# Optimization experiments

Hardware: AMD Instinct MI355X
Metric: run time of the kernel (lower is better)

## Reference

```python
import jax, jax.numpy as jnp
import numpy as np

N = 65536          # number of atoms (routing tokens)
NUM_SPECIES = 4    # number of per-species expert models
D_IN, D_HID, D_OUT = 256, 1024, 256


def setup_inputs() -> dict:
    key = jax.random.key(0)
    k = jax.random.split(key, 6)
    x = jax.random.normal(k[0], (N, D_IN), dtype=jnp.float32)
    central_species = jax.random.randint(k[1], (N,), 0, NUM_SPECIES, dtype=jnp.int64)
    # Per-species 2-layer MLP experts, stacked along species axis.
    W1 = jax.random.normal(k[2], (NUM_SPECIES, D_IN, D_HID), dtype=jnp.float32) * (1.0 / np.sqrt(D_IN))
    b1 = jnp.zeros((NUM_SPECIES, D_HID), dtype=jnp.float32)
    W2 = jax.random.normal(k[3], (NUM_SPECIES, D_HID, D_OUT), dtype=jnp.float32) * (1.0 / np.sqrt(D_HID))
    b2 = jnp.zeros((NUM_SPECIES, D_OUT), dtype=jnp.float32)
    return {"x": x, "central_species": central_species, "W1": W1, "b1": b1, "W2": W2, "b2": b2}


def reference(x, central_species, W1, b1, W2, b2):
    # Equivalent to: split rows by species (CentralSplitter), apply the
    # species-specific submodel, scatter results back by mask (CentralUniter).
    # Dense-compute-and-select expression: every row receives exactly the
    # output of its own species' expert, identical math to masked gather/scatter.
    num_species = W1.shape[0]
    out = jnp.zeros((x.shape[0], W2.shape[-1]), dtype=x.dtype)
    for s in range(num_species):  # small fixed expert count
        h = jax.nn.silu(x @ W1[s] + b1[s])          # [N, D_HID]
        y = h @ W2[s] + b2[s]                       # [N, D_OUT]
        sel = (central_species == s)[:, None]
        out = out + jnp.where(sel, y, jnp.zeros_like(y))
    return out
```

## Files before the change

kernel.cpp:

```cpp
#include <hip/hip_runtime.h>
#include <hip/hip_bf16.h>


#define N_ATOMS 65536
#define D_IN 256
#define D_HID 1024
#define D_OUT 256
#define TPS 1024

typedef __attribute__((ext_vector_type(8))) short short8;
typedef __attribute__((ext_vector_type(4))) short short4v;
typedef __attribute__((ext_vector_type(4))) float float4e;
typedef __attribute__((ext_vector_type(2))) unsigned uint2e;
typedef __attribute__((ext_vector_type(4))) unsigned uint4e;

#define WS_BUCKET_OFF 256
#define WS_W1_OFF 1048832
#define WS_W2_OFF 3145984

__device__ __forceinline__ short f2bf(float f) {
  unsigned u = __builtin_bit_cast(unsigned, f);
  unsigned r = (u + 0x7FFFu + ((u >> 16) & 1u)) >> 16;
  return (short)r;
}

__device__ __forceinline__ unsigned cvt_pk_bf16(float a, float b) {
  unsigned r;
  asm("v_cvt_pk_bf16_f32 %0, %1, %2" : "=v"(r) : "v"(a), "v"(b));
  return r;
}

__global__ void prep_kernel(const float* __restrict__ W1, const float* __restrict__ W2,
                            short* __restrict__ w1sw, short* __restrict__ w2sw,
                            int* __restrict__ cnt) {
  int gid = blockIdx.x * 256 + threadIdx.x;
  if (gid < 64) cnt[gid] = 0;
  int lane = gid & 63;
  int lr = lane & 15;
  int lk = (lane >> 4) * 8;
  if (gid < 131072) {
    int ks = (gid >> 6) & 7;
    int nt = (gid >> 9) & 63;
    int s  = gid >> 15;
    const float* src = W1 + ((size_t)(s * 256 + ks * 32 + lk)) * 1024 + nt * 16 + lr;
    short8 v;
    for (int j = 0; j < 8; ++j) v[j] = f2bf(src[(size_t)j * 1024]);
    *(short8*)(w1sw + (size_t)gid * 8) = v;
  } else {
    int g = gid - 131072;
    int kt = (g >> 6) & 31;
    int nt = (g >> 11) & 15;
    int s  = g >> 15;
    const float* src = W2 + ((size_t)(s * 1024 + kt * 32 + lk)) * 256 + nt * 16 + lr;
    short8 v;
    for (int j = 0; j < 8; ++j) v[j] = f2bf(src[(size_t)j * 256]);
    *(short8*)(w2sw + (size_t)g * 8) = v;
  }
}

#define CF_BLOCKS 32
#define CF_ITERS 8
__global__ void count_fill_kernel(const int* __restrict__ species,
                                  int* __restrict__ cnt, int* __restrict__ bucket) {
  int tid = threadIdx.x;
  int lane = tid & 63, wid = tid >> 6;
  __shared__ int wcnt[CF_ITERS][4][4];
  __shared__ int wb[CF_ITERS][4][4];
  __shared__ int base_sm[4];
  int sv[CF_ITERS], rk[CF_ITERS];
  unsigned long long below = (1ull << lane) - 1ull;
  int base_i = blockIdx.x * (CF_ITERS * 256);
  #pragma unroll
  for (int it = 0; it < CF_ITERS; ++it) {
    int s = species[base_i + it * 256 + tid] & 3;
    sv[it] = s;
    unsigned long long m0 = __ballot(s == 0);
    unsigned long long m1 = __ballot(s == 1);
    unsigned long long m2 = __ballot(s == 2);
    unsigned long long m3 = __ballot(s == 3);
    unsigned long long ms = (s == 0) ? m0 : (s == 1) ? m1 : (s == 2) ? m2 : m3;
    rk[it] = __popcll(ms & below);
    if (lane == 0) {
      wcnt[it][wid][0] = __popcll(m0);
      wcnt[it][wid][1] = __popcll(m1);
      wcnt[it][wid][2] = __popcll(m2);
      wcnt[it][wid][3] = __popcll(m3);
    }
  }
  __syncthreads();
  if (tid < 4) {
    int ss = tid, run = 0;
    for (int it = 0; it < CF_ITERS; ++it)
      for (int w = 0; w < 4; ++w) {
        wb[it][w][ss] = run;
        run += wcnt[it][w][ss];
      }
    base_sm[ss] = atomicAdd(&cnt[ss * 16], run);
  }
  __syncthreads();
  #pragma unroll
  for (int it = 0; it < CF_ITERS; ++it) {
    int ss = sv[it];
    bucket[ss * N_ATOMS + base_sm[ss] + wb[it][wid][ss] + rk[it]] = base_i + it * 256 + tid;
  }
}

#define XS_STRIDE 280
#define HS_STRIDE 152
__global__ __launch_bounds__(256, 2) void fused_kernel(
    const float* __restrict__ x, const int* __restrict__ cntArr,
    const int* __restrict__ bucket, const short* __restrict__ w1sw,
    const short* __restrict__ w2sw, const float* __restrict__ b1,
    const float* __restrict__ b2, float* __restrict__ out) {
  int bid = blockIdx.x;
  int s = (bid & 7) >> 1;
  int t = ((bid >> 3) << 1) | (bid & 1);
  int cnt = cntArr[s * 16];
  int r0 = t * 64;
  if (r0 >= cnt) return;
  int nrows = min(64, cnt - r0);
  const int* buck = bucket + s * N_ATOMS + r0;

  __shared__ short Xs[64 * XS_STRIDE];
  __shared__ short Hs[2][64 * HS_STRIDE];

  int tid = threadIdx.x;

  for (int i = 0; i < 8; ++i) {
    int id = tid + i * 256;
    int r = id >> 5;
    int g = id & 31;
    float4 f0 = {}, f1 = {};
    if (r < nrows) {
      const float4* src = (const float4*)(x + (size_t)buck[r] * D_IN + g * 8);
      f0 = src[0];
      f1 = src[1];
    }
    uint4e v;
    v.x = cvt_pk_bf16(f0.x, f0.y);
    v.y = cvt_pk_bf16(f0.z, f0.w);
    v.z = cvt_pk_bf16(f1.x, f1.y);
    v.w = cvt_pk_bf16(f1.z, f1.w);
    *(uint4e*)(Xs + r * XS_STRIDE + g * 8) = v;
  }

  int lane = tid & 63;
  int wid = tid >> 6;
  int lr = lane & 15;
  int lk = (lane >> 4) * 8;
  int lq = (lane >> 4) * 4;

  int rowIdx[4];
  #pragma unroll
  for (int bt = 0; bt < 4; ++bt) {
    int r = bt * 16 + lr;
    rowIdx[bt] = (r < nrows) ? buck[r] : -1;
  }

  float4e accY[4][4];
  #pragma unroll
  for (int at = 0; at < 4; ++at) {
    float4e bv = *(const float4e*)(b2 + s * D_OUT + wid * 64 + at * 16 + lq);
    #pragma unroll
    for (int bt = 0; bt < 4; ++bt) accY[at][bt] = bv;
  }

  short8 b1f[16];
  #pragma unroll
  for (int ks = 0; ks < 8; ++ks)
    #pragma unroll
    for (int at = 0; at < 2; ++at) {
      int nt = 0 * 8 + wid * 2 + at;
      b1f[ks * 2 + at] = *(const short8*)(w1sw + ((size_t)((s * 64 + nt) * 8 + ks)) * 512 + lane * 8);
    }

  __syncthreads();

  for (int c = 0; c < 8; ++c) {
    float4e acc1[2][4];
    #pragma unroll
    for (int at = 0; at < 2; ++at) {
      float4e bv = *(const float4e*)(b1 + s * D_HID + c * 128 + wid * 32 + at * 16 + lq);
      #pragma unroll
      for (int bt = 0; bt < 4; ++bt) acc1[at][bt] = bv;
    }
    __builtin_amdgcn_s_setprio(1);
    #pragma unroll
    for (int ks = 0; ks < 8; ++ks) {
      short8 xb[4];
      #pragma unroll
      for (int bt = 0; bt < 4; ++bt)
        xb[bt] = *(const short8*)(Xs + (bt * 16 + lr) * XS_STRIDE + ks * 32 + lk);
      #pragma unroll
      for (int at = 0; at < 2; ++at)
        #pragma unroll
        for (int bt = 0; bt < 4; ++bt)
          acc1[at][bt] = __builtin_amdgcn_mfma_f32_16x16x32_bf16(b1f[ks * 2 + at], xb[bt], acc1[at][bt], 0, 0, 0);
    }
    __builtin_amdgcn_s_setprio(0);
    short8 b2f[16];
    #pragma unroll
    for (int ks = 0; ks < 4; ++ks)
      #pragma unroll
      for (int at = 0; at < 4; ++at) {
        int nt = wid * 4 + at;
        int kt = c * 4 + ks;
        b2f[ks * 4 + at] = *(const short8*)(w2sw + ((size_t)((s * 16 + nt) * 32 + kt)) * 512 + lane * 8);
      }
    short* hsb = Hs[c & 1];
    #pragma unroll
    for (int at = 0; at < 2; ++at) {
      int hidloc = wid * 32 + at * 16 + lq;
      #pragma unroll
      for (int bt = 0; bt < 4; ++bt) {
        float4e v4 = acc1[at][bt];
        float sv0 = v4[0] * __builtin_amdgcn_rcpf(1.0f + __expf(-v4[0]));
        float sv1 = v4[1] * __builtin_amdgcn_rcpf(1.0f + __expf(-v4[1]));
        float sv2 = v4[2] * __builtin_amdgcn_rcpf(1.0f + __expf(-v4[2]));
        float sv3 = v4[3] * __builtin_amdgcn_rcpf(1.0f + __expf(-v4[3]));
        uint2e h;
        h.x = cvt_pk_bf16(sv0, sv1);
        h.y = cvt_pk_bf16(sv2, sv3);
        *(uint2e*)(hsb + (bt * 16 + lr) * HS_STRIDE + hidloc) = h;
      }
    }
    __syncthreads();
    if (c < 7) {
      #pragma unroll
      for (int ks = 0; ks < 8; ++ks)
        #pragma unroll
        for (int at = 0; at < 2; ++at) {
          int nt = (c + 1) * 8 + wid * 2 + at;
          b1f[ks * 2 + at] = *(const short8*)(w1sw + ((size_t)((s * 64 + nt) * 8 + ks)) * 512 + lane * 8);
        }
    }
    __builtin_amdgcn_s_setprio(1);
    #pragma unroll
    for (int ks = 0; ks < 4; ++ks) {
      short8 hb[4];
      #pragma unroll
      for (int bt = 0; bt < 4; ++bt)
        hb[bt] = *(const short8*)(hsb + (bt * 16 + lr) * HS_STRIDE + ks * 32 + lk);
      #pragma unroll
      for (int at = 0; at < 4; ++at)
        #pragma unroll
        for (int bt = 0; bt < 4; ++bt)
          accY[at][bt] = __builtin_amdgcn_mfma_f32_16x16x32_bf16(b2f[ks * 4 + at], hb[bt], accY[at][bt], 0, 0, 0);
    }
    __builtin_amdgcn_s_setprio(0);
  }

  #pragma unroll
  for (int at = 0; at < 4; ++at) {
    int nb = wid * 64 + at * 16 + lq;
    #pragma unroll
    for (int bt = 0; bt < 4; ++bt) {
      if (rowIdx[bt] >= 0)
        *(float4e*)(out + (size_t)rowIdx[bt] * D_OUT + nb) = accY[at][bt];
    }
  }
}

extern "C" void kernel_launch(void* const* d_in, const int* in_sizes, int n_in,
                              void* d_out, int out_size, void* d_ws, size_t ws_size,
                              hipStream_t stream) {
  const float* x  = (const float*)d_in[0];
  const int* spc  = (const int*)d_in[1];
  const float* W1 = (const float*)d_in[2];
  const float* b1 = (const float*)d_in[3];
  const float* W2 = (const float*)d_in[4];
  const float* b2 = (const float*)d_in[5];
  float* out = (float*)d_out;

  int*   cnt    = (int*)d_ws;
  int*   bucket = (int*)((char*)d_ws + WS_BUCKET_OFF);
  short* w1sw   = (short*)((char*)d_ws + WS_W1_OFF);
  short* w2sw   = (short*)((char*)d_ws + WS_W2_OFF);

  prep_kernel<<<1024, 256, 0, stream>>>(W1, W2, w1sw, w2sw, cnt);
  count_fill_kernel<<<CF_BLOCKS, 256, 0, stream>>>(spc, cnt, bucket);
  fused_kernel<<<4 * TPS, 256, 0, stream>>>(x, cnt, bucket, w1sw, w2sw, b1, b2, out);
}
```

Before: 219.9 us.

## Merge weight prep and species bucketing into one kernel launch

```diff
diff --git a/kernel.cpp b/kernel.cpp
--- a/kernel.cpp
+++ b/kernel.cpp
@@ -9,7 +9,6 @@
 #define TPS 1024
 
 typedef __attribute__((ext_vector_type(8))) short short8;
-typedef __attribute__((ext_vector_type(4))) short short4v;
 typedef __attribute__((ext_vector_type(4))) float float4e;
 typedef __attribute__((ext_vector_type(2))) unsigned uint2e;
 typedef __attribute__((ext_vector_type(4))) unsigned uint4e;
@@ -17,6 +16,10 @@
 #define WS_BUCKET_OFF 256
 #define WS_W1_OFF 1048832
 #define WS_W2_OFF 3145984
+
+#define CF_BLOCKS 32
+#define CF_ITERS 8
+#define CF_ROWS (CF_ITERS * 256)
 
 __device__ __forceinline__ short f2bf(float f) {
   unsigned u = __builtin_bit_cast(unsigned, f);
@@ -30,11 +33,77 @@
   return r;
 }
 
-__global__ void prep_kernel(const float* __restrict__ W1, const float* __restrict__ W2,
-                            short* __restrict__ w1sw, short* __restrict__ w2sw,
-                            int* __restrict__ cnt) {
-  int gid = blockIdx.x * 256 + threadIdx.x;
-  if (gid < 64) cnt[gid] = 0;
+__global__ __launch_bounds__(256) void prep_count_kernel(
+    const float* __restrict__ W1, const float* __restrict__ W2,
+    short* __restrict__ w1sw, short* __restrict__ w2sw,
+    const int* __restrict__ species, int* __restrict__ cnt,
+    int* __restrict__ bucket) {
+  int tid = threadIdx.x;
+
+  if (blockIdx.x < CF_BLOCKS) {
+    __shared__ int red[4];
+    __shared__ int wcnt[CF_ITERS][4][4];
+    __shared__ int wb[CF_ITERS][4][4];
+    int b = blockIdx.x;
+    if (tid < 4) red[tid] = 0;
+    __syncthreads();
+
+    int pc0 = 0, pc1 = 0, pc2 = 0, pc3 = 0;
+    int nPrefix = b * CF_ROWS;
+    for (int base = tid * 4; base < nPrefix; base += 1024) {
+      int4 v = *(const int4*)(species + base);
+      int s0 = v.x & 3, s1 = v.y & 3, s2 = v.z & 3, s3 = v.w & 3;
+      pc0 += (s0 == 0) + (s1 == 0) + (s2 == 0) + (s3 == 0);
+      pc1 += (s0 == 1) + (s1 == 1) + (s2 == 1) + (s3 == 1);
+      pc2 += (s0 == 2) + (s1 == 2) + (s2 == 2) + (s3 == 2);
+      pc3 += (s0 == 3) + (s1 == 3) + (s2 == 3) + (s3 == 3);
+    }
+    if (pc0) atomicAdd(&red[0], pc0);
+    if (pc1) atomicAdd(&red[1], pc1);
+    if (pc2) atomicAdd(&red[2], pc2);
+    if (pc3) atomicAdd(&red[3], pc3);
+
+    int lane = tid & 63, wid = tid >> 6;
+    int sv[CF_ITERS], rk[CF_ITERS];
+    unsigned long long below = (1ull << lane) - 1ull;
+    int base_i = b * CF_ROWS;
+    #pragma unroll
+    for (int it = 0; it < CF_ITERS; ++it) {
+      int s = species[base_i + it * 256 + tid] & 3;
+      sv[it] = s;
+      unsigned long long m0 = __ballot(s == 0);
+      unsigned long long m1 = __ballot(s == 1);
+      unsigned long long m2 = __ballot(s == 2);
+      unsigned long long m3 = __ballot(s == 3);
+      unsigned long long ms = (s == 0) ? m0 : (s == 1) ? m1 : (s == 2) ? m2 : m3;
+      rk[it] = __popcll(ms & below);
+      if (lane == 0) {
+        wcnt[it][wid][0] = __popcll(m0);
+        wcnt[it][wid][1] = __popcll(m1);
+        wcnt[it][wid][2] = __popcll(m2);
+        wcnt[it][wid][3] = __popcll(m3);
+      }
+    }
+    __syncthreads();
+    if (tid < 4) {
+      int ss = tid, run = 0;
+      for (int it = 0; it < CF_ITERS; ++it)
+        for (int w = 0; w < 4; ++w) {
+          wb[it][w][ss] = run;
+          run += wcnt[it][w][ss];
+        }
+      if (b == CF_BLOCKS - 1) cnt[ss * 16] = red[ss] + run;
+    }
+    __syncthreads();
+    #pragma unroll
+    for (int it = 0; it < CF_ITERS; ++it) {
+      int ss = sv[it];
+      bucket[ss * N_ATOMS + red[ss] + wb[it][wid][ss] + rk[it]] = base_i + it * 256 + tid;
+    }
+    return;
+  }
+
+  int gid = (blockIdx.x - CF_BLOCKS) * 256 + tid;
   int lane = gid & 63;
   int lr = lane & 15;
   int lk = (lane >> 4) * 8;
@@ -58,53 +127,6 @@
   }
 }
 
-#define CF_BLOCKS 32
-#define CF_ITERS 8
-__global__ void count_fill_kernel(const int* __restrict__ species,
-                                  int* __restrict__ cnt, int* __restrict__ bucket) {
-  int tid = threadIdx.x;
-  int lane = tid & 63, wid = tid >> 6;
-  __shared__ int wcnt[CF_ITERS][4][4];
-  __shared__ int wb[CF_ITERS][4][4];
-  __shared__ int base_sm[4];
-  int sv[CF_ITERS], rk[CF_ITERS];
-  unsigned long long below = (1ull << lane) - 1ull;
-  int base_i = blockIdx.x * (CF_ITERS * 256);
-  #pragma unroll
-  for (int it = 0; it < CF_ITERS; ++it) {
-    int s = species[base_i + it * 256 + tid] & 3;
-    sv[it] = s;
-    unsigned long long m0 = __ballot(s == 0);
-    unsigned long long m1 = __ballot(s == 1);
-    unsigned long long m2 = __ballot(s == 2);
-    unsigned long long m3 = __ballot(s == 3);
-    unsigned long long ms = (s == 0) ? m0 : (s == 1) ? m1 : (s == 2) ? m2 : m3;
-    rk[it] = __popcll(ms & below);
-    if (lane == 0) {
-      wcnt[it][wid][0] = __popcll(m0);
-      wcnt[it][wid][1] = __popcll(m1);
-      wcnt[it][wid][2] = __popcll(m2);
-      wcnt[it][wid][3] = __popcll(m3);
-    }
-  }
-  __syncthreads();
-  if (tid < 4) {
-    int ss = tid, run = 0;
-    for (int it = 0; it < CF_ITERS; ++it)
-      for (int w = 0; w < 4; ++w) {
-        wb[it][w][ss] = run;
-        run += wcnt[it][w][ss];
-      }
-    base_sm[ss] = atomicAdd(&cnt[ss * 16], run);
-  }
-  __syncthreads();
-  #pragma unroll
-  for (int it = 0; it < CF_ITERS; ++it) {
-    int ss = sv[it];
-    bucket[ss * N_ATOMS + base_sm[ss] + wb[it][wid][ss] + rk[it]] = base_i + it * 256 + tid;
-  }
-}
-
 #define XS_STRIDE 280
 #define HS_STRIDE 152
 __global__ __launch_bounds__(256, 2) void fused_kernel(
@@ -277,7 +299,6 @@
   short* w1sw   = (short*)((char*)d_ws + WS_W1_OFF);
   short* w2sw   = (short*)((char*)d_ws + WS_W2_OFF);
 
-  prep_kernel<<<1024, 256, 0, stream>>>(W1, W2, w1sw, w2sw, cnt);
-  count_fill_kernel<<<CF_BLOCKS, 256, 0, stream>>>(spc, cnt, bucket);
+  prep_count_kernel<<<CF_BLOCKS + 1024, 256, 0, stream>>>(W1, W2, w1sw, w2sw, spc, cnt, bucket);
   fused_kernel<<<4 * TPS, 256, 0, stream>>>(x, cnt, bucket, w1sw, w2sw, b1, b2, out);
 }
```

Measured after the change: 232.4 us. +5.7%, slower.

## Switch expert MLP to 32x32x16 bf16 MFMA tiles with matching weight swizzle

Applied to the files above, without the earlier changes.

```diff
diff --git a/kernel.cpp b/kernel.cpp
--- a/kernel.cpp
+++ b/kernel.cpp
@@ -9,8 +9,8 @@
 #define TPS 1024
 
 typedef __attribute__((ext_vector_type(8))) short short8;
-typedef __attribute__((ext_vector_type(4))) short short4v;
 typedef __attribute__((ext_vector_type(4))) float float4e;
+typedef __attribute__((ext_vector_type(16))) float f32x16;
 typedef __attribute__((ext_vector_type(2))) unsigned uint2e;
 typedef __attribute__((ext_vector_type(4))) unsigned uint4e;
 
@@ -36,30 +36,30 @@
   int gid = blockIdx.x * 256 + threadIdx.x;
   if (gid < 64) cnt[gid] = 0;
   int lane = gid & 63;
-  int lr = lane & 15;
-  int lk = (lane >> 4) * 8;
+  int lc = lane & 31;
+  int lk = (lane >> 5) * 8;
   if (gid < 131072) {
-    int ks = (gid >> 6) & 7;
-    int nt = (gid >> 9) & 63;
+    int kt = (gid >> 6) & 15;
+    int nt = (gid >> 10) & 31;
     int s  = gid >> 15;
-    const float* src = W1 + ((size_t)(s * 256 + ks * 32 + lk)) * 1024 + nt * 16 + lr;
+    const float* src = W1 + ((size_t)(s * 256 + kt * 16 + lk)) * 1024 + nt * 32 + lc;
     short8 v;
     for (int j = 0; j < 8; ++j) v[j] = f2bf(src[(size_t)j * 1024]);
     *(short8*)(w1sw + (size_t)gid * 8) = v;
   } else {
     int g = gid - 131072;
-    int kt = (g >> 6) & 31;
-    int nt = (g >> 11) & 15;
+    int kt = (g >> 6) & 63;
+    int nt = (g >> 12) & 7;
     int s  = g >> 15;
-    const float* src = W2 + ((size_t)(s * 1024 + kt * 32 + lk)) * 256 + nt * 16 + lr;
+    const float* src = W2 + ((size_t)(s * 1024 + kt * 16 + lk)) * 256 + nt * 32 + lc;
     short8 v;
     for (int j = 0; j < 8; ++j) v[j] = f2bf(src[(size_t)j * 256]);
     *(short8*)(w2sw + (size_t)g * 8) = v;
   }
 }
 
-#define CF_BLOCKS 32
-#define CF_ITERS 8
+#define CF_BLOCKS 8
+#define CF_ITERS 32
 __global__ void count_fill_kernel(const int* __restrict__ species,
                                   int* __restrict__ cnt, int* __restrict__ bucket) {
   int tid = threadIdx.x;
@@ -146,117 +146,127 @@
 
   int lane = tid & 63;
   int wid = tid >> 6;
-  int lr = lane & 15;
-  int lk = (lane >> 4) * 8;
-  int lq = (lane >> 4) * 4;
-
-  int rowIdx[4];
-  #pragma unroll
-  for (int bt = 0; bt < 4; ++bt) {
-    int r = bt * 16 + lr;
+  int lr = lane & 31;
+  int hk = lane >> 5;
+  int lk = hk * 8;
+
+  int rowIdx[2];
+  #pragma unroll
+  for (int bt = 0; bt < 2; ++bt) {
+    int r = bt * 32 + lr;
     rowIdx[bt] = (r < nrows) ? buck[r] : -1;
   }
 
-  float4e accY[4][4];
-  #pragma unroll
-  for (int at = 0; at < 4; ++at) {
-    float4e bv = *(const float4e*)(b2 + s * D_OUT + wid * 64 + at * 16 + lq);
-    #pragma unroll
-    for (int bt = 0; bt < 4; ++bt) accY[at][bt] = bv;
+  f32x16 accY[2][2];
+  #pragma unroll
+  for (int ot = 0; ot < 2; ++ot) {
+    #pragma unroll
+    for (int g = 0; g < 4; ++g) {
+      float4e bv = *(const float4e*)(b2 + s * D_OUT + wid * 64 + ot * 32 + g * 8 + hk * 4);
+      #pragma unroll
+      for (int q = 0; q < 4; ++q) {
+        accY[ot][0][g * 4 + q] = bv[q];
+        accY[ot][1][g * 4 + q] = bv[q];
+      }
+    }
   }
 
   short8 b1f[16];
   #pragma unroll
-  for (int ks = 0; ks < 8; ++ks)
-    #pragma unroll
-    for (int at = 0; at < 2; ++at) {
-      int nt = 0 * 8 + wid * 2 + at;
-      b1f[ks * 2 + at] = *(const short8*)(w1sw + ((size_t)((s * 64 + nt) * 8 + ks)) * 512 + lane * 8);
-    }
+  for (int kt = 0; kt < 16; ++kt) {
+    int nt = 0 * 4 + wid;
+    b1f[kt] = *(const short8*)(w1sw + ((size_t)((s * 32 + nt) * 16 + kt)) * 512 + lane * 8);
+  }
 
   __syncthreads();
 
   for (int c = 0; c < 8; ++c) {
-    float4e acc1[2][4];
-    #pragma unroll
-    for (int at = 0; at < 2; ++at) {
-      float4e bv = *(const float4e*)(b1 + s * D_HID + c * 128 + wid * 32 + at * 16 + lq);
-      #pragma unroll
-      for (int bt = 0; bt < 4; ++bt) acc1[at][bt] = bv;
+    f32x16 acc1[2];
+    #pragma unroll
+    for (int g = 0; g < 4; ++g) {
+      float4e bv = *(const float4e*)(b1 + s * D_HID + c * 128 + wid * 32 + g * 8 + hk * 4);
+      #pragma unroll
+      for (int q = 0; q < 4; ++q) {
+        acc1[0][g * 4 + q] = bv[q];
+        acc1[1][g * 4 + q] = bv[q];
+      }
     }
     __builtin_amdgcn_s_setprio(1);
     #pragma unroll
-    for (int ks = 0; ks < 8; ++ks) {
-      short8 xb[4];
-      #pragma unroll
-      for (int bt = 0; bt < 4; ++bt)
-        xb[bt] = *(const short8*)(Xs + (bt * 16 + lr) * XS_STRIDE + ks * 32 + lk);
-      #pragma unroll
-      for (int at = 0; at < 2; ++at)
-        #pragma unroll
-        for (int bt = 0; bt < 4; ++bt)
-          acc1[at][bt] = __builtin_amdgcn_mfma_f32_16x16x32_bf16(b1f[ks * 2 + at], xb[bt], acc1[at][bt], 0, 0, 0);
+    for (int kt = 0; kt < 16; ++kt) {
+      short8 xb[2];
+      #pragma unroll
+      for (int bt = 0; bt < 2; ++bt)
+        xb[bt] = *(const short8*)(Xs + (bt * 32 + lr) * XS_STRIDE + kt * 16 + lk);
+      #pragma unroll
+      for (int bt = 0; bt < 2; ++bt)
+        acc1[bt] = __builtin_amdgcn_mfma_f32_32x32x16_bf16(b1f[kt], xb[bt], acc1[bt], 0, 0, 0);
     }
     __builtin_amdgcn_s_setprio(0);
     short8 b2f[16];
     #pragma unroll
-    for (int ks = 0; ks < 4; ++ks)
-      #pragma unroll
-      for (int at = 0; at < 4; ++at) {
-        int nt = wid * 4 + at;
-        int kt = c * 4 + ks;
-        b2f[ks * 4 + at] = *(const short8*)(w2sw + ((size_t)((s * 16 + nt) * 32 + kt)) * 512 + lane * 8);
+    for (int kt = 0; kt < 8; ++kt)
+      #pragma unroll
+      for (int ot = 0; ot < 2; ++ot) {
+        int nt = wid * 2 + ot;
+        b2f[kt * 2 + ot] = *(const short8*)(w2sw + ((size_t)((s * 8 + nt) * 64 + c * 8 + kt)) * 512 + lane * 8);
       }
     short* hsb = Hs[c & 1];
     #pragma unroll
-    for (int at = 0; at < 2; ++at) {
-      int hidloc = wid * 32 + at * 16 + lq;
-      #pragma unroll
-      for (int bt = 0; bt < 4; ++bt) {
-        float4e v4 = acc1[at][bt];
-        float sv0 = v4[0] * __builtin_amdgcn_rcpf(1.0f + __expf(-v4[0]));
-        float sv1 = v4[1] * __builtin_amdgcn_rcpf(1.0f + __expf(-v4[1]));
-        float sv2 = v4[2] * __builtin_amdgcn_rcpf(1.0f + __expf(-v4[2]));
-        float sv3 = v4[3] * __builtin_amdgcn_rcpf(1.0f + __expf(-v4[3]));
+    for (int bt = 0; bt < 2; ++bt) {
+      #pragma unroll
+      for (int g = 0; g < 4; ++g) {
+        float p0 = acc1[bt][g * 4 + 0], p1 = acc1[bt][g * 4 + 1];
+        float p2 = acc1[bt][g * 4 + 2], p3 = acc1[bt][g * 4 + 3];
+        float sv0 = p0 * __builtin_amdgcn_rcpf(1.0f + __expf(-p0));
+        float sv1 = p1 * __builtin_amdgcn_rcpf(1.0f + __expf(-p1));
+        float sv2 = p2 * __builtin_amdgcn_rcpf(1.0f + __expf(-p2));
+        float sv3 = p3 * __builtin_amdgcn_rcpf(1.0f + __expf(-p3));
         uint2e h;
         h.x = cvt_pk_bf16(sv0, sv1);
         h.y = cvt_pk_bf16(sv2, sv3);
-        *(uint2e*)(hsb + (bt * 16 + lr) * HS_STRIDE + hidloc) = h;
+        *(uint2e*)(hsb + (bt * 32 + lr) * HS_STRIDE + wid * 32 + g * 8 + hk * 4) = h;
       }
     }
     __syncthreads();
     if (c < 7) {
       #pragma unroll
-      for (int ks = 0; ks < 8; ++ks)
+      for (int kt = 0; kt < 16; ++kt) {
+        int nt = (c + 1) * 4 + wid;
+        b1f[kt] = *(const short8*)(w1sw + ((size_t)((s * 32 + nt) * 16 + kt)) * 512 + lane * 8);
+      }
+    }
+    __builtin_amdgcn_s_setprio(1);
+    #pragma unroll
+    for (int kt = 0; kt < 8; ++kt) {
+      short8 hb[2];
+      #pragma unroll
+      for (int bt = 0; bt < 2; ++bt)
+        hb[bt] = *(const short8*)(hsb + (bt * 32 + lr) * HS_STRIDE + kt * 16 + lk);
+      #pragma unroll
+      for (int ot = 0; ot < 2; ++ot)
         #pragma unroll
-        for (int at = 0; at < 2; ++at) {
-          int nt = (c + 1) * 8 + wid * 2 + at;
-          b1f[ks * 2 + at] = *(const short8*)(w1sw + ((size_t)((s * 64 + nt) * 8 + ks)) * 512 + lane * 8);
+        for (int bt = 0; bt < 2; ++bt)
+          accY[ot][bt] = __builtin_amdgcn_mfma_f32_32x32x16_bf16(b2f[kt * 2 + ot], hb[bt], accY[ot][bt], 0, 0, 0);
+    }
+    __builtin_amdgcn_s_setprio(0);
+  }
+
+  #pragma unroll
+  for (int ot = 0; ot < 2; ++ot) {
+    #pragma unroll
+    for (int bt = 0; bt < 2; ++bt) {
+      if (rowIdx[bt] >= 0) {
+        #pragma unroll
+        for (int g = 0; g < 4; ++g) {
+          float4e o;
+          o[0] = accY[ot][bt][g * 4 + 0];
+          o[1] = accY[ot][bt][g * 4 + 1];
+          o[2] = accY[ot][bt][g * 4 + 2];
+          o[3] = accY[ot][bt][g * 4 + 3];
+          *(float4e*)(out + (size_t)rowIdx[bt] * D_OUT + wid * 64 + ot * 32 + g * 8 + hk * 4) = o;
         }
-    }
-    __builtin_amdgcn_s_setprio(1);
-    #pragma unroll
-    for (int ks = 0; ks < 4; ++ks) {
-      short8 hb[4];
-      #pragma unroll
-      for (int bt = 0; bt < 4; ++bt)
-        hb[bt] = *(const short8*)(hsb + (bt * 16 + lr) * HS_STRIDE + ks * 32 + lk);
-      #pragma unroll
-      for (int at = 0; at < 4; ++at)
-        #pragma unroll
-        for (int bt = 0; bt < 4; ++bt)
-          accY[at][bt] = __builtin_amdgcn_mfma_f32_16x16x32_bf16(b2f[ks * 4 + at], hb[bt], accY[at][bt], 0, 0, 0);
-    }
-    __builtin_amdgcn_s_setprio(0);
-  }
-
-  #pragma unroll
-  for (int at = 0; at < 4; ++at) {
-    int nb = wid * 64 + at * 16 + lq;
-    #pragma unroll
-    for (int bt = 0; bt < 4; ++bt) {
-      if (rowIdx[bt] >= 0)
-        *(float4e*)(out + (size_t)rowIdx[bt] * D_OUT + nb) = accY[at][bt];
+      }
     }
   }
 }
```

After: 232.7 us. +5.8%, slower.
